# Kernel optimization log

Measured on AMD Instinct MI355X. Metric: run time of the kernel, lower is better.

Reference implementation:

```python
import jax, jax.numpy as jnp
import numpy as np

B, L, H, DH, DM, DFF, V, NL, NP, NT = 4, 2048, 12, 64, 768, 3072, 30522, 12, 2048, 2
LN_EPS = 1e-5       # fast_transformers default LayerNorm eps
EMB_LN_EPS = 1e-12  # BERT embeddings LayerNorm eps
ATT_EPS = 1e-6      # linear attention normalizer eps


def layer_norm(x, w, b, eps):
    m = jnp.mean(x, axis=-1, keepdims=True)
    v = jnp.mean((x - m) ** 2, axis=-1, keepdims=True)
    return (x - m) * jax.lax.rsqrt(v + eps) * w + b


def setup_inputs() -> dict:
    key = jax.random.key(0)
    ks = jax.random.split(key, 24)
    s = 0.02
    d = {
        "input_ids": jax.random.randint(ks[0], (B, L), 0, V),
        "attention_mask": jnp.ones((B, L), jnp.float32),
        "token_type_ids": jnp.zeros((B, L), jnp.int64),
        "word_emb": jax.random.normal(ks[1], (V, DM), jnp.float32) * s,
        "pos_emb": jax.random.normal(ks[2], (NP, DM), jnp.float32) * s,
        "type_emb": jax.random.normal(ks[3], (NT, DM), jnp.float32) * s,
        "emb_ln_w": jnp.ones((DM,), jnp.float32),
        "emb_ln_b": jnp.zeros((DM,), jnp.float32),
        "Wq": jax.random.normal(ks[4], (NL, DM, DM), jnp.float32) * s,
        "bq": jnp.zeros((NL, DM), jnp.float32),
        "Wk": jax.random.normal(ks[5], (NL, DM, DM), jnp.float32) * s,
        "bk": jnp.zeros((NL, DM), jnp.float32),
        "Wv": jax.random.normal(ks[6], (NL, DM, DM), jnp.float32) * s,
        "bv": jnp.zeros((NL, DM), jnp.float32),
        "Wo": jax.random.normal(ks[7], (NL, DM, DM), jnp.float32) * s,
        "bo": jnp.zeros((NL, DM), jnp.float32),
        "ln1_w": jnp.ones((NL, DM), jnp.float32),
        "ln1_b": jnp.zeros((NL, DM), jnp.float32),
        "W1": jax.random.normal(ks[8], (NL, DFF, DM), jnp.float32) * s,
        "b1": jnp.zeros((NL, DFF), jnp.float32),
        "W2": jax.random.normal(ks[9], (NL, DM, DFF), jnp.float32) * s,
        "b2": jnp.zeros((NL, DM), jnp.float32),
        "ln2_w": jnp.ones((NL, DM), jnp.float32),
        "ln2_b": jnp.zeros((NL, DM), jnp.float32),
    }
    return d


def _encoder(x, mask, Wq, bq, Wk, bk, Wv, bv, Wo, bo, ln1_w, ln1_b, W1, b1, W2, b2, ln2_w, ln2_b):
    b, l = x.shape[:2]
    for i in range(NL):
        # linear attention (fast_transformers): phi = elu + 1
        q = (x @ Wq[i].T + bq[i]).reshape(b, l, H, DH)
        k = (x @ Wk[i].T + bk[i]).reshape(b, l, H, DH)
        v = (x @ Wv[i].T + bv[i]).reshape(b, l, H, DH)
        Q = jax.nn.elu(q) + 1.0
        K = (jax.nn.elu(k) + 1.0) * mask[:, :, None, None]  # zero padded keys
        KV = jnp.einsum('nshd,nshm->nhmd', K, v)            # [b,H,DH(m=val),DH(d=key)]
        Z = 1.0 / (jnp.einsum('nlhd,nhd->nlh', Q, K.sum(axis=1)) + ATT_EPS)
        a = jnp.einsum('nlhd,nhmd,nlh->nlhm', Q, KV, Z).reshape(b, l, DM)
        a = a @ Wo[i].T + bo[i]
        x = layer_norm(x + a, ln1_w[i], ln1_b[i], LN_EPS)
        y = jax.nn.gelu(x @ W1[i].T + b1[i], approximate=False)
        y = y @ W2[i].T + b2[i]
        x = layer_norm(x + y, ln2_w[i], ln2_b[i], LN_EPS)
    return x


def reference(input_ids, attention_mask, token_type_ids, word_emb, pos_emb, type_emb,
              emb_ln_w, emb_ln_b, Wq, bq, Wk, bk, Wv, bv, Wo, bo,
              ln1_w, ln1_b, W1, b1, W2, b2, ln2_w, ln2_b):
    b, l = input_ids.shape
    e = word_emb[input_ids] + pos_emb[:l][None, :, :] + type_emb[token_type_ids]
    x = layer_norm(e, emb_ln_w, emb_ln_b, EMB_LN_EPS)
    return _encoder(x, attention_mask, Wq, bq, Wk, bk, Wv, bv, Wo, bo,
                    ln1_w, ln1_b, W1, b1, W2, b2, ln2_w, ln2_b)
```

## Files before the change

kernel.cpp:

```cpp
#include <hip/hip_runtime.h>
#include <math.h>

#define B_   4
#define L_   2048
#define H_   12
#define DH_  64
#define DM_  768
#define DFF_ 3072
#define NL_  12
#define M_   (B_*L_)
#define NCH_ 32
#define QLD_ 2304
#define LN_EPS_  1e-5f
#define EMB_EPS_ 1e-12f
#define ATT_EPS_ 1e-6f

typedef unsigned short u16;
typedef __bf16 bf16x8 __attribute__((ext_vector_type(8)));
typedef float  f32x4  __attribute__((ext_vector_type(4)));

__device__ __forceinline__ u16 f2b(float f) {
  unsigned u = __builtin_bit_cast(unsigned, f);
  u += 0x7fffu + ((u >> 16) & 1u);
  return (u16)(u >> 16);
}
__device__ __forceinline__ float b2f(u16 s) {
  return __builtin_bit_cast(float, (unsigned)((unsigned)s << 16));
}
__device__ __forceinline__ float wredsum(float v) {
  #pragma unroll
  for (int o = 32; o > 0; o >>= 1) v += __shfl_xor(v, o, 64);
  return v;
}
__device__ __forceinline__ void gld16(const void* g, void* l) {
  __builtin_amdgcn_global_load_lds(
      (const __attribute__((address_space(1))) void*)g,
      (__attribute__((address_space(3))) void*)l, 16, 0, 0);
}

__global__ __launch_bounds__(256) void cvt_bf16(const float* __restrict__ in,
                                                u16* __restrict__ out, int n4) {
  int i = blockIdx.x * 256 + threadIdx.x;
  if (i >= n4) return;
  float4 f = ((const float4*)in)[i];
  ushort4 o;
  o.x = f2b(f.x); o.y = f2b(f.y); o.z = f2b(f.z); o.w = f2b(f.w);
  ((ushort4*)out)[i] = o;
}

__global__ __launch_bounds__(256) void cvt_bf16_qkv(const float* __restrict__ in,
                                                    u16* __restrict__ out, int ro) {
  int i = blockIdx.x * 256 + threadIdx.x;
  if (i >= NL_*DM_*DM_/4) return;
  int row = i / 192;
  int c4  = (i % 192) * 4;
  int l = row / DM_, r = row % DM_;
  float4 f = ((const float4*)in)[i];
  ushort4 o;
  o.x = f2b(f.x); o.y = f2b(f.y); o.z = f2b(f.z); o.w = f2b(f.w);
  *(ushort4*)(out + ((size_t)l*QLD_ + ro + r)*DM_ + c4) = o;
}

__global__ __launch_bounds__(256) void fuse_bias(const float* __restrict__ bq,
    const float* __restrict__ bk, const float* __restrict__ bv, float* __restrict__ out) {
  int i = blockIdx.x * 256 + threadIdx.x;
  if (i >= NL_*QLD_) return;
  int l = i / QLD_, r = i % QLD_;
  float v = r < DM_ ? bq[l*DM_ + r] : r < 2*DM_ ? bk[l*DM_ + r - DM_] : bv[l*DM_ + r - 2*DM_];
  out[i] = v;
}

__global__ __launch_bounds__(256) void embed_ln(
    const int* __restrict__ ids, const int* __restrict__ tts,
    const float* __restrict__ we, const float* __restrict__ pe,
    const float* __restrict__ te, const float* __restrict__ lw,
    const float* __restrict__ lb, float* __restrict__ x32, u16* __restrict__ xb)
{
  int row  = blockIdx.x * 4 + (threadIdx.x >> 6);
  int lane = threadIdx.x & 63;
  int l  = row & (L_ - 1);
  int id = ids[row];
  int tt = tts[row];
  const float* wr = we + (size_t)id * DM_;
  const float* pr = pe + (size_t)l  * DM_;
  const float* tr = te + (size_t)tt * DM_;
  float v[12]; float s = 0.f;
  #pragma unroll
  for (int j = 0; j < 12; j++) { int c = j*64 + lane; v[j] = wr[c] + pr[c] + tr[c]; s += v[j]; }
  s = wredsum(s);
  float m = s * (1.f/768.f);
  float q = 0.f;
  #pragma unroll
  for (int j = 0; j < 12; j++) { float d = v[j] - m; q += d*d; }
  q = wredsum(q);
  float rs = rsqrtf(q * (1.f/768.f) + EMB_EPS_);
  float* xo = x32 + (size_t)row * DM_;
  u16*   bo = xb  + (size_t)row * DM_;
  #pragma unroll
  for (int j = 0; j < 12; j++) {
    int c = j*64 + lane;
    float o = (v[j] - m) * rs * lw[c] + lb[c];
    xo[c] = o; bo[c] = f2b(o);
  }
}

__global__ __launch_bounds__(256) void ln_res(
    float* __restrict__ x32, const float* __restrict__ t32,
    const float* __restrict__ lw, const float* __restrict__ lb,
    u16* __restrict__ xb, float eps)
{
  int row  = blockIdx.x * 4 + (threadIdx.x >> 6);
  int lane = threadIdx.x & 63;
  float* xr = x32 + (size_t)row * DM_;
  const float* tr = t32 + (size_t)row * DM_;
  float v[12]; float s = 0.f;
  #pragma unroll
  for (int j = 0; j < 12; j++) { int c = j*64 + lane; v[j] = xr[c] + tr[c]; s += v[j]; }
  s = wredsum(s);
  float m = s * (1.f/768.f);
  float q = 0.f;
  #pragma unroll
  for (int j = 0; j < 12; j++) { float d = v[j] - m; q += d*d; }
  q = wredsum(q);
  float rs = rsqrtf(q * (1.f/768.f) + eps);
  u16* bo = xb + (size_t)row * DM_;
  #pragma unroll
  for (int j = 0; j < 12; j++) {
    int c = j*64 + lane;
    float o = (v[j] - m) * rs * lw[c] + lb[c];
    xr[c] = o; bo[c] = f2b(o);
  }
}

template<int EPI>
__global__ __launch_bounds__(256)
void gemm_gl(const u16* __restrict__ A, const u16* __restrict__ Bw,
             const float* __restrict__ bias,
             u16* __restrict__ Co, float* __restrict__ Cf,
             int M, int N, int K, int ldc)
{
  __shared__ alignas(16) u16 sA[128*64];
  __shared__ alignas(16) u16 sB[128*64];
  const int tid  = threadIdx.x;
  const int lane = tid & 63;
  const int w    = tid >> 6;
  const int wr = w >> 1, wc = w & 1;
  const int row0 = blockIdx.x * 128;
  const int col0 = blockIdx.y * 128;
  const int lr = lane & 15;
  const int g  = lane >> 4;
  const int srow = lane >> 3;
  const int acol = (((lane & 7) ^ srow) * 8);

  f32x4 acc[4][4];
  #pragma unroll
  for (int i = 0; i < 4; i++)
    #pragma unroll
    for (int j = 0; j < 4; j++) acc[i][j] = (f32x4){0.f,0.f,0.f,0.f};

  const u16* Ap = A  + (size_t)row0 * K;
  const u16* Bp = Bw + (size_t)col0 * K;

  for (int kt = 0; kt < K; kt += 64) {
    #pragma unroll
    for (int j = 0; j < 4; j++) {
      gld16(Ap + (size_t)(w*32 + j*8 + srow)*K + kt + acol, sA + (w*32 + j*8)*64);
      gld16(Bp + (size_t)(w*32 + j*8 + srow)*K + kt + acol, sB + (w*32 + j*8)*64);
    }
    __syncthreads();
    #pragma unroll
    for (int kk = 0; kk < 2; kk++) {
      const int gg = ((kk*4 + g) ^ (lr & 7)) * 8;
      bf16x8 af[4], bv[4];
      #pragma unroll
      for (int m = 0; m < 4; m++) af[m] = *(const bf16x8*)(sA + (wr*64 + m*16 + lr)*64 + gg);
      #pragma unroll
      for (int n = 0; n < 4; n++) bv[n] = *(const bf16x8*)(sB + (wc*64 + n*16 + lr)*64 + gg);
      #pragma unroll
      for (int m = 0; m < 4; m++)
        #pragma unroll
        for (int n = 0; n < 4; n++)
          acc[m][n] = __builtin_amdgcn_mfma_f32_16x16x32_bf16(af[m], bv[n], acc[m][n], 0, 0, 0);
    }
    __syncthreads();
  }

  #pragma unroll
  for (int m = 0; m < 4; m++) {
    const int row_b = row0 + wr*64 + m*16 + (lane >> 4) * 4;
    #pragma unroll
    for (int n = 0; n < 4; n++) {
      const int col = col0 + wc*64 + n*16 + lr;
      const float bvb = bias[col];
      #pragma unroll
      for (int r = 0; r < 4; r++) {
        float v = acc[m][n][r] + bvb;
        if constexpr (EPI == 4) { if (col < 2*DM_) v = v > 0.f ? v + 1.f : expf(v); }
        if constexpr (EPI == 2) v = 0.5f * v * (1.f + erff(v * 0.70710678118654752f));
        const size_t off = (size_t)(row_b + r) * ldc + col;
        if constexpr (EPI == 3) Cf[off] = v;
        else                    Co[off] = f2b(v);
      }
    }
  }
}

__global__ __launch_bounds__(256)
void gemm_n64(const u16* __restrict__ A, const u16* __restrict__ Bw,
              const float* __restrict__ bias, float* __restrict__ Cf,
              int M, int N, int K, int ldc)
{
  __shared__ alignas(16) u16 sA[128*64];
  __shared__ alignas(16) u16 sB[64*64];
  const int tid  = threadIdx.x;
  const int lane = tid & 63;
  const int w    = tid >> 6;
  const int row0 = blockIdx.x * 128;
  const int col0 = blockIdx.y * 64;
  const int lr = lane & 15;
  const int g  = lane >> 4;
  const int srow = lane >> 3;
  const int acol = (((lane & 7) ^ srow) * 8);

  f32x4 acc[2][4];
  #pragma unroll
  for (int i = 0; i < 2; i++)
    #pragma unroll
    for (int j = 0; j < 4; j++) acc[i][j] = (f32x4){0.f,0.f,0.f,0.f};

  const u16* ApA = A  + (size_t)(row0)*K;
  const u16* BpB = Bw + (size_t)(col0)*K;

  for (int kt = 0; kt < K; kt += 64) {
    #pragma unroll
    for (int j = 0; j < 4; j++)
      gld16(ApA + (size_t)(w*32 + j*8 + srow)*K + kt + acol, sA + (w*32 + j*8)*64);
    #pragma unroll
    for (int j = 0; j < 2; j++)
      gld16(BpB + (size_t)(w*16 + j*8 + srow)*K + kt + acol, sB + (w*16 + j*8)*64);
    __syncthreads();
    #pragma unroll
    for (int kk = 0; kk < 2; kk++) {
      bf16x8 af[2], bv[4];
      #pragma unroll
      for (int m = 0; m < 2; m++) {
        const int R = w*32 + m*16 + lr;
        const int gg = (kk*4 + g) ^ (lr & 7);
        af[m] = *(const bf16x8*)(sA + R*64 + gg*8);
      }
      #pragma unroll
      for (int n = 0; n < 4; n++) {
        const int R = n*16 + lr;
        const int gg = (kk*4 + g) ^ (lr & 7);
        bv[n] = *(const bf16x8*)(sB + R*64 + gg*8);
      }
      #pragma unroll
      for (int m = 0; m < 2; m++)
        #pragma unroll
        for (int n = 0; n < 4; n++)
          acc[m][n] = __builtin_amdgcn_mfma_f32_16x16x32_bf16(af[m], bv[n], acc[m][n], 0, 0, 0);
    }
    __syncthreads();
  }

  #pragma unroll
  for (int m = 0; m < 2; m++) {
    const int row_b = row0 + w*32 + m*16 + (lane >> 4) * 4;
    #pragma unroll
    for (int n = 0; n < 4; n++) {
      const int col = col0 + n*16 + lr;
      const float bvb = bias[col];
      #pragma unroll
      for (int r = 0; r < 4; r++)
        Cf[(size_t)(row_b + r) * ldc + col] = acc[m][n][r] + bvb;
    }
  }
}

__global__ __launch_bounds__(256) void kv_part(
    const u16* __restrict__ qkv, const float* __restrict__ mask,
    float* __restrict__ kvp, float* __restrict__ ksp)
{
  __shared__ float sK[64*64];
  __shared__ float sV[64*64];
  const int bh = blockIdx.x;
  const int b = bh / H_, h = bh % H_;
  const int s0 = blockIdx.y * 64;
  const int t = threadIdx.x;
  const u16* kb = qkv + DM_;
  const u16* vb = qkv + 2*DM_;
  #pragma unroll
  for (int r = 0; r < 2; r++) {
    int idx = r*256 + t;
    int sr = idx >> 3;
    int c  = (idx & 7) * 8;
    int sg = s0 + sr;
    size_t base = ((size_t)(b*L_ + sg)) * QLD_ + h*DH_ + c;
    uint4 kk = *(const uint4*)(kb + base);
    uint4 vv = *(const uint4*)(vb + base);
    float mk = mask[b*L_ + sg];
    const u16* kp = (const u16*)&kk;
    const u16* vp = (const u16*)&vv;
    #pragma unroll
    for (int j = 0; j < 8; j++) {
      sK[sr*64 + c + j] = b2f(kp[j]) * mk;
      sV[sr*64 + c + j] = b2f(vp[j]);
    }
  }
  __syncthreads();
  const int m0 = (t >> 4) * 4;
  const int d0 = (t & 15) * 4;
  float acc[4][4] = {{0.f}};
  float ks[4] = {0.f, 0.f, 0.f, 0.f};
  for (int s = 0; s < 64; s++) {
    float4 vm = *(const float4*)(sV + s*64 + m0);
    float4 kk = *(const float4*)(sK + s*64 + d0);
    float vmv[4] = {vm.x, vm.y, vm.z, vm.w};
    float kkv[4] = {kk.x, kk.y, kk.z, kk.w};
    #pragma unroll
    for (int i = 0; i < 4; i++)
      #pragma unroll
      for (int j = 0; j < 4; j++) acc[i][j] += vmv[i] * kkv[j];
    if (t < 16) { ks[0] += kkv[0]; ks[1] += kkv[1]; ks[2] += kkv[2]; ks[3] += kkv[3]; }
  }
  float* o = kvp + ((size_t)bh*NCH_ + blockIdx.y) * 4096;
  #pragma unroll
  for (int i = 0; i < 4; i++) {
    float4 wv = {acc[i][0], acc[i][1], acc[i][2], acc[i][3]};
    *(float4*)(o + (m0 + i)*64 + d0) = wv;
  }
  if (t < 16) {
    float* ko = ksp + ((size_t)bh*NCH_ + blockIdx.y) * 64;
    #pragma unroll
    for (int j = 0; j < 4; j++) ko[d0 + j] = ks[j];
  }
}

__global__ __launch_bounds__(256) void kv_reduce(
    const float* __restrict__ kvp, const float* __restrict__ ksp,
    float* __restrict__ kv, float* __restrict__ ksum)
{
  const int bh = blockIdx.x;
  const int i = blockIdx.y * 256 + threadIdx.x;
  float s = 0.f;
  #pragma unroll 8
  for (int c = 0; c < NCH_; c++) s += kvp[((size_t)bh*NCH_ + c)*4096 + i];
  kv[(size_t)bh*4096 + i] = s;
  if (blockIdx.y == 0 && threadIdx.x < 64) {
    float q = 0.f;
    #pragma unroll 8
    for (int c = 0; c < NCH_; c++) q += ksp[((size_t)bh*NCH_ + c)*64 + threadIdx.x];
    ksum[bh*64 + threadIdx.x] = q;
  }
}

__global__ __launch_bounds__(256) void attn_av(
    const u16* __restrict__ qkv, const float* __restrict__ kv,
    const float* __restrict__ ksum, u16* __restrict__ ab)
{
  __shared__ alignas(16) u16 sQ[128*72];
  __shared__ alignas(16) u16 sKV[64*72];
  __shared__ float sKs[64];
  __shared__ float sZ[128];
  const int bh = blockIdx.x;
  const int b = bh / H_, h = bh % H_;
  const int l0 = blockIdx.y * 128;
  const int t = threadIdx.x;
  const int lane = t & 63;
  const int w = t >> 6;
  for (int i = t; i < 4096; i += 256)
    sKV[(i >> 6)*72 + (i & 63)] = f2b(kv[(size_t)bh*4096 + i]);
  if (t < 64) sKs[t] = ksum[bh*64 + t];
  #pragma unroll
  for (int r = 0; r < 4; r++) {
    int idx = r*256 + t;
    int s = idx >> 3;
    int c = (idx & 7) * 8;
    *(uint4*)(sQ + s*72 + c) =
        *(const uint4*)(qkv + ((size_t)(b*L_ + l0 + s)) * QLD_ + h*DH_ + c);
  }
  __syncthreads();
  {
    int row = t >> 1, half = t & 1;
    float zd = 0.f;
    #pragma unroll
    for (int ch = 0; ch < 4; ch++) {
      bf16x8 qv = *(const bf16x8*)(sQ + row*72 + half*32 + ch*8);
      #pragma unroll
      for (int j = 0; j < 8; j++) zd += (float)qv[j] * sKs[half*32 + ch*8 + j];
    }
    zd += __shfl_xor(zd, 1, 64);
    if (half == 0) sZ[row] = 1.f / (zd + ATT_EPS_);
  }
  const int lr = lane & 15, lk = (lane >> 4) * 8;
  f32x4 acc[2][4];
  #pragma unroll
  for (int m = 0; m < 2; m++)
    #pragma unroll
    for (int n = 0; n < 4; n++) acc[m][n] = (f32x4){0.f,0.f,0.f,0.f};
  #pragma unroll
  for (int kk = 0; kk < 2; kk++) {
    bf16x8 af[2], bv[4];
    #pragma unroll
    for (int m = 0; m < 2; m++) af[m] = *(const bf16x8*)(sQ + (w*32 + m*16 + lr)*72 + kk*32 + lk);
    #pragma unroll
    for (int n = 0; n < 4; n++) bv[n] = *(const bf16x8*)(sKV + (n*16 + lr)*72 + kk*32 + lk);
    #pragma unroll
    for (int m = 0; m < 2; m++)
      #pragma unroll
      for (int n = 0; n < 4; n++)
        acc[m][n] = __builtin_amdgcn_mfma_f32_16x16x32_bf16(af[m], bv[n], acc[m][n], 0, 0, 0);
  }
  __syncthreads();
  #pragma unroll
  for (int m = 0; m < 2; m++) {
    const int row_l = w*32 + m*16 + (lane >> 4) * 4;
    #pragma unroll
    for (int n = 0; n < 4; n++) {
      const int col = n*16 + lr;
      #pragma unroll
      for (int r = 0; r < 4; r++) {
        float v = acc[m][n][r] * sZ[row_l + r];
        ab[((size_t)(b*L_ + l0 + row_l + r)) * DM_ + h*DH_ + col] = f2b(v);
      }
    }
  }
}

__global__ __launch_bounds__(256) void copyf4(const float4* __restrict__ in,
                                              float4* __restrict__ out, int n4) {
  int i = blockIdx.x * 256 + threadIdx.x;
  if (i < n4) out[i] = in[i];
}

extern "C" void kernel_launch(void* const* d_in, const int* in_sizes, int n_in,
                              void* d_out, int out_size, void* d_ws, size_t ws_size,
                              hipStream_t stream)
{
  const int*   ids  = (const int*)d_in[0];
  const float* mask = (const float*)d_in[1];
  const int*   tts  = (const int*)d_in[2];
  const float* we   = (const float*)d_in[3];
  const float* pe   = (const float*)d_in[4];
  const float* te   = (const float*)d_in[5];
  const float* elw  = (const float*)d_in[6];
  const float* elb  = (const float*)d_in[7];
  const float* Wq   = (const float*)d_in[8];
  const float* bq   = (const float*)d_in[9];
  const float* Wk   = (const float*)d_in[10];
  const float* bk   = (const float*)d_in[11];
  const float* Wv   = (const float*)d_in[12];
  const float* bv   = (const float*)d_in[13];
  const float* Wo   = (const float*)d_in[14];
  const float* bo   = (const float*)d_in[15];
  const float* l1w  = (const float*)d_in[16];
  const float* l1b  = (const float*)d_in[17];
  const float* W1   = (const float*)d_in[18];
  const float* b1   = (const float*)d_in[19];
  const float* W2   = (const float*)d_in[20];
  const float* b2   = (const float*)d_in[21];
  const float* l2w  = (const float*)d_in[22];
  const float* l2b  = (const float*)d_in[23];

  char* p = (char*)d_ws;
  auto alloc = [&](size_t n) -> char* {
    char* r = p; p += (n + 255) & ~(size_t)255; return r;
  };
  const size_t SQ = (size_t)NL_ * DM_ * DM_;
  const size_t SF = (size_t)NL_ * DFF_ * DM_;
  u16*  wqkvb = (u16*)alloc((size_t)NL_ * QLD_ * DM_ * 2);
  u16*  wob   = (u16*)alloc(SQ * 2);
  u16*  w1b   = (u16*)alloc(SF * 2);
  u16*  w2b   = (u16*)alloc(SF * 2);
  float* bqkv = (float*)alloc((size_t)NL_ * QLD_ * 4);
  float* x32  = (float*)alloc((size_t)M_ * DM_ * 4);
  float* t32  = (float*)alloc((size_t)M_ * DM_ * 4);
  u16*  xb    = (u16*)alloc((size_t)M_ * DM_ * 2);
  u16*  qkv   = (u16*)alloc((size_t)M_ * QLD_ * 2);
  u16*  abuf  = (u16*)alloc((size_t)M_ * DM_ * 2);
  u16*  ybuf  = (u16*)alloc((size_t)M_ * DFF_ * 2);
  float* kvb  = (float*)alloc((size_t)(B_*H_*DH_*DH_ + B_*H_*DH_) * 4);
  float* ksm  = kvb + (size_t)B_*H_*DH_*DH_;
  float* ksp  = (float*)alloc((size_t)B_*H_*NCH_*DH_ * 4);
  float* kvp  = t32;

  const int nq4 = (int)(SQ/4);
  cvt_bf16_qkv<<<(nq4+255)/256, 256, 0, stream>>>(Wq, wqkvb, 0);
  cvt_bf16_qkv<<<(nq4+255)/256, 256, 0, stream>>>(Wk, wqkvb, DM_);
  cvt_bf16_qkv<<<(nq4+255)/256, 256, 0, stream>>>(Wv, wqkvb, 2*DM_);
  cvt_bf16<<<nq4/256, 256, 0, stream>>>(Wo, wob, nq4);
  cvt_bf16<<<(int)(SF/4/256), 256, 0, stream>>>(W1, w1b, (int)(SF/4));
  cvt_bf16<<<(int)(SF/4/256), 256, 0, stream>>>(W2, w2b, (int)(SF/4));
  fuse_bias<<<(NL_*QLD_+255)/256, 256, 0, stream>>>(bq, bk, bv, bqkv);

  embed_ln<<<M_/4, 256, 0, stream>>>(ids, tts, we, pe, te, elw, elb, x32, xb);

  for (int il = 0; il < NL_; ++il) {
    const u16* wqkv = wqkvb + (size_t)il * QLD_ * DM_;
    const u16* wo = wob + (size_t)il * DM_ * DM_;
    const u16* w1 = w1b + (size_t)il * DFF_ * DM_;
    const u16* w2 = w2b + (size_t)il * DFF_ * DM_;

    gemm_gl<4><<<dim3(M_/128, QLD_/128), 256, 0, stream>>>(
        xb, wqkv, bqkv + (size_t)il*QLD_, qkv, nullptr, M_, QLD_, DM_, QLD_);

    kv_part<<<dim3(B_*H_, NCH_), 256, 0, stream>>>(qkv, mask, kvp, ksp);
    kv_reduce<<<dim3(B_*H_, 16), 256, 0, stream>>>(kvp, ksp, kvb, ksm);
    attn_av<<<dim3(B_*H_, L_/128), 256, 0, stream>>>(qkv, kvb, ksm, abuf);

    gemm_n64<<<dim3(M_/128, DM_/64), 256, 0, stream>>>(
        abuf, wo, bo + (size_t)il*DM_, t32, M_, DM_, DM_, DM_);
    ln_res<<<M_/4, 256, 0, stream>>>(x32, t32, l1w + (size_t)il*DM_, l1b + (size_t)il*DM_, xb, LN_EPS_);

    gemm_gl<2><<<dim3(M_/128, DFF_/128), 256, 0, stream>>>(
        xb, w1, b1 + (size_t)il*DFF_, ybuf, nullptr, M_, DFF_, DM_, DFF_);
    gemm_n64<<<dim3(M_/128, DM_/64), 256, 0, stream>>>(
        ybuf, w2, b2 + (size_t)il*DM_, t32, M_, DM_, DFF_, DM_);
    ln_res<<<M_/4, 256, 0, stream>>>(x32, t32, l2w + (size_t)il*DM_, l2b + (size_t)il*DM_, xb, LN_EPS_);
  }

  copyf4<<<(M_*DM_/4)/256, 256, 0, stream>>>((const float4*)x32, (float4*)d_out, M_*DM_/4);
}
```

Baseline: 3.227 ms.

## Double-buffer LDS tiles in bf16 GEMM kernels to overlap loads with MFMA

Both GEMM kernels (gemm_gl and gemm_n64) now use two LDS buffers for each of the A and B tiles. The next K-tile is issued into the spare buffer before the MFMA loop runs on the current one, which removes one barrier per iteration and aims to hide global-load latency behind compute. The cost is twice the LDS per block (64 KB for gemm_gl), which can cut how many blocks fit on a CU and so reduce the latency hiding that came from occupancy. The swizzled index is also hoisted out of the inner loops in gemm_n64.

```diff
diff --git a/kernel.cpp b/kernel.cpp
--- a/kernel.cpp
+++ b/kernel.cpp
@@ -139,8 +139,10 @@
              u16* __restrict__ Co, float* __restrict__ Cf,
              int M, int N, int K, int ldc)
 {
-  __shared__ alignas(16) u16 sA[128*64];
-  __shared__ alignas(16) u16 sB[128*64];
+  __shared__ alignas(16) u16 sA0[128*64];
+  __shared__ alignas(16) u16 sA1[128*64];
+  __shared__ alignas(16) u16 sB0[128*64];
+  __shared__ alignas(16) u16 sB1[128*64];
   const int tid  = threadIdx.x;
   const int lane = tid & 63;
   const int w    = tid >> 6;
@@ -161,21 +163,34 @@
   const u16* Ap = A  + (size_t)row0 * K;
   const u16* Bp = Bw + (size_t)col0 * K;
 
-  for (int kt = 0; kt < K; kt += 64) {
+  auto STAGE = [&](u16* dA, u16* dB, int kt) {
     #pragma unroll
     for (int j = 0; j < 4; j++) {
-      gld16(Ap + (size_t)(w*32 + j*8 + srow)*K + kt + acol, sA + (w*32 + j*8)*64);
-      gld16(Bp + (size_t)(w*32 + j*8 + srow)*K + kt + acol, sB + (w*32 + j*8)*64);
-    }
-    __syncthreads();
+      gld16(Ap + (size_t)(w*32 + j*8 + srow)*K + kt + acol, dA + (w*32 + j*8)*64);
+      gld16(Bp + (size_t)(w*32 + j*8 + srow)*K + kt + acol, dB + (w*32 + j*8)*64);
+    }
+  };
+
+  const int nt = K >> 6;
+  STAGE(sA0, sB0, 0);
+  __syncthreads();
+
+  for (int t = 0; t < nt; ++t) {
+    u16* rA = (t & 1) ? sA1 : sA0;
+    u16* rB = (t & 1) ? sB1 : sB0;
+    if (t + 1 < nt) {
+      u16* dA = (t & 1) ? sA0 : sA1;
+      u16* dB = (t & 1) ? sB0 : sB1;
+      STAGE(dA, dB, (t + 1) * 64);
+    }
     #pragma unroll
     for (int kk = 0; kk < 2; kk++) {
       const int gg = ((kk*4 + g) ^ (lr & 7)) * 8;
       bf16x8 af[4], bv[4];
       #pragma unroll
-      for (int m = 0; m < 4; m++) af[m] = *(const bf16x8*)(sA + (wr*64 + m*16 + lr)*64 + gg);
-      #pragma unroll
-      for (int n = 0; n < 4; n++) bv[n] = *(const bf16x8*)(sB + (wc*64 + n*16 + lr)*64 + gg);
+      for (int m = 0; m < 4; m++) af[m] = *(const bf16x8*)(rA + (wr*64 + m*16 + lr)*64 + gg);
+      #pragma unroll
+      for (int n = 0; n < 4; n++) bv[n] = *(const bf16x8*)(rB + (wc*64 + n*16 + lr)*64 + gg);
       #pragma unroll
       for (int m = 0; m < 4; m++)
         #pragma unroll
@@ -210,8 +225,10 @@
               const float* __restrict__ bias, float* __restrict__ Cf,
               int M, int N, int K, int ldc)
 {
-  __shared__ alignas(16) u16 sA[128*64];
-  __shared__ alignas(16) u16 sB[64*64];
+  __shared__ alignas(16) u16 sA0[128*64];
+  __shared__ alignas(16) u16 sA1[128*64];
+  __shared__ alignas(16) u16 sB0[64*64];
+  __shared__ alignas(16) u16 sB1[64*64];
   const int tid  = threadIdx.x;
   const int lane = tid & 63;
   const int w    = tid >> 6;
@@ -231,29 +248,35 @@
   const u16* ApA = A  + (size_t)(row0)*K;
   const u16* BpB = Bw + (size_t)(col0)*K;
 
-  for (int kt = 0; kt < K; kt += 64) {
+  auto STAGE = [&](u16* dA, u16* dB, int kt) {
     #pragma unroll
     for (int j = 0; j < 4; j++)
-      gld16(ApA + (size_t)(w*32 + j*8 + srow)*K + kt + acol, sA + (w*32 + j*8)*64);
+      gld16(ApA + (size_t)(w*32 + j*8 + srow)*K + kt + acol, dA + (w*32 + j*8)*64);
     #pragma unroll
     for (int j = 0; j < 2; j++)
-      gld16(BpB + (size_t)(w*16 + j*8 + srow)*K + kt + acol, sB + (w*16 + j*8)*64);
-    __syncthreads();
+      gld16(BpB + (size_t)(w*16 + j*8 + srow)*K + kt + acol, dB + (w*16 + j*8)*64);
+  };
+
+  const int nt = K >> 6;
+  STAGE(sA0, sB0, 0);
+  __syncthreads();
+
+  for (int t = 0; t < nt; ++t) {
+    u16* rA = (t & 1) ? sA1 : sA0;
+    u16* rB = (t & 1) ? sB1 : sB0;
+    if (t + 1 < nt) {
+      u16* dA = (t & 1) ? sA0 : sA1;
+      u16* dB = (t & 1) ? sB0 : sB1;
+      STAGE(dA, dB, (t + 1) * 64);
+    }
     #pragma unroll
     for (int kk = 0; kk < 2; kk++) {
+      const int gg = ((kk*4 + g) ^ (lr & 7)) * 8;
       bf16x8 af[2], bv[4];
       #pragma unroll
-      for (int m = 0; m < 2; m++) {
-        const int R = w*32 + m*16 + lr;
-        const int gg = (kk*4 + g) ^ (lr & 7);
-        af[m] = *(const bf16x8*)(sA + R*64 + gg*8);
-      }
-      #pragma unroll
-      for (int n = 0; n < 4; n++) {
-        const int R = n*16 + lr;
-        const int gg = (kk*4 + g) ^ (lr & 7);
-        bv[n] = *(const bf16x8*)(sB + R*64 + gg*8);
-      }
+      for (int m = 0; m < 2; m++) af[m] = *(const bf16x8*)(rA + (w*32 + m*16 + lr)*64 + gg);
+      #pragma unroll
+      for (int n = 0; n < 4; n++) bv[n] = *(const bf16x8*)(rB + (n*16 + lr)*64 + gg);
       #pragma unroll
       for (int m = 0; m < 2; m++)
         #pragma unroll
```

Result: no change. 3.263 ms (+1.1%).
